# Kernel optimization log

Hardware: AMD Instinct MI355X
Metric: run time of the kernel (lower is better)

Reference implementation:

```python
import jax, jax.numpy as jnp
import numpy as np

B, T, D_IN, H, S, DH = 128, 256, 512, 1024, 128, 1024

def _lin(key, out_d, in_d):
    k = 1.0 / np.sqrt(in_d)
    return jax.random.uniform(key, (out_d, in_d), jnp.float32, -k, k)

def setup_inputs() -> dict:
    key = jax.random.key(0)
    ks = jax.random.split(key, 16)
    kH = 1.0 / np.sqrt(H)
    return {
        'x': jax.random.normal(ks[0], (B, T, D_IN), jnp.float32),
        'noise': jax.random.normal(ks[1], (B, T, S), jnp.float32),
        # LSTM (torch gate order: i, f, g, o)
        'W_ih': _lin(ks[2], 4 * H, S),
        'W_hh': _lin(ks[3], 4 * H, H),
        'b_ih': jax.random.uniform(ks[4], (4 * H,), jnp.float32, -kH, kH),
        'b_hh': jax.random.uniform(ks[5], (4 * H,), jnp.float32, -kH, kH),
        # posterior heads over concat(x_t, h_t): in = H + D_IN
        'Wm': _lin(ks[6], S, H + D_IN), 'bm': jnp.zeros((S,), jnp.float32),
        'Wv': _lin(ks[7], S, H + D_IN), 'bv': jnp.zeros((S,), jnp.float32),
        # decoder MLP
        'Wd1': _lin(ks[8], DH, S), 'bd1': jnp.zeros((DH,), jnp.float32),
        'Wd2': _lin(ks[9], D_IN, DH), 'bd2': jnp.zeros((D_IN,), jnp.float32),
    }

def reference(x, noise, W_ih, W_hh, b_ih, b_hh, Wm, bm, Wv, bv, Wd1, bd1, Wd2, bd2):
    Bb = x.shape[0]
    Hh = W_hh.shape[1]
    Ss = Wm.shape[0]
    dt = x.dtype

    def step(carry, inp):
        h, c, z = carry          # [B,H], [B,H], [B,S]
        xt, nt = inp             # [B,D_IN], [B,S]
        gates = z @ W_ih.T + b_ih + h @ W_hh.T + b_hh   # [B,4H]
        i, f, g, o = jnp.split(gates, 4, axis=-1)
        c = jax.nn.sigmoid(f) * c + jax.nn.sigmoid(i) * jnp.tanh(g)
        h = jax.nn.sigmoid(o) * jnp.tanh(c)
        pi = jnp.concatenate([xt, h], axis=-1)           # [B, D_IN+H]
        mean = pi @ Wm.T + bm
        log_var = pi @ Wv.T + bv
        std = jnp.exp(0.5 * log_var)
        z_new = nt * std + mean
        kl = jnp.sum(std * std + mean * mean - jnp.log(std) - 0.5)
        return (h, c, z_new), (z_new, kl)

    init = (jnp.zeros((Bb, Hh), dt), jnp.zeros((Bb, Hh), dt), jnp.zeros((Bb, Ss), dt))
    xs = (jnp.swapaxes(x, 0, 1), jnp.swapaxes(noise, 0, 1))  # time-major
    _, (zs, kls) = jax.lax.scan(step, init, xs)
    z = jnp.swapaxes(zs, 0, 1)                                # [B,T,S]
    kl = jnp.sum(kls)
    x_hat = jax.nn.relu(z @ Wd1.T + bd1) @ Wd2.T + bd2        # [B,T,D_IN]
    return x_hat, kl
```

## Files before the change

### kernel.cpp

```cpp
#include <hip/hip_runtime.h>
#include <hip/hip_bf16.h>

#define Bdim 128
#define Tdim 256
#define DIN 512
#define Hdim 1024
#define Sdim 128
#define DHdim 1024
#define KG 1152
#define KP 1536
#define NBLK 192

using short8  = __attribute__((ext_vector_type(8))) short;
using floatx4 = __attribute__((ext_vector_type(4))) float;
typedef unsigned long long ull;

#define MFMA(a, b, c) __builtin_amdgcn_mfma_f32_16x16x32_bf16((a), (b), (c), 0, 0, 0)

#define XBF_OFF   0ull
#define WG_OFF    33554432ull
#define WMV_OFF   42991616ull
#define HB_OFF    0ull
#define WD1_OFF   67108864ull
#define WD2_OFF   67371008ull
#define AB_OFF    68419584ull
#define AB_SZ     294912ull
#define ZALL_OFF  69009408ull
#define KL_OFF    77398016ull
#define FLG_OFF   77398144ull

__device__ __forceinline__ float sigf(float v) { return 1.0f / (1.0f + __expf(-v)); }
__device__ __forceinline__ float tanhfast(float v) { return 1.0f - 2.0f / (__expf(2.0f * v) + 1.0f); }

__device__ __forceinline__ short8 cload16(const __hip_bfloat16* p) {
  short8 r;
  asm volatile("global_load_dwordx4 %0, %1, off sc0 sc1" : "=&v"(r) : "v"(p));
  return r;
}
#define VMWAIT0()                                              \
  do {                                                         \
    asm volatile("s_waitcnt vmcnt(0)" ::: "memory");           \
    __builtin_amdgcn_sched_barrier(0);                         \
  } while (0)
#define CFENCE() asm volatile("" ::: "memory")

__device__ __forceinline__ void astore8(__hip_bfloat16* p, ull v) {
  __hip_atomic_store((ull*)(void*)p, v, __ATOMIC_RELAXED, __HIP_MEMORY_SCOPE_AGENT);
}

__device__ __forceinline__ void waitflags(unsigned* flags, int base, int mask,
                                          unsigned target, int lane) {
  unsigned* p = flags + base + (lane & mask);
  while (!__all((int)(__hip_atomic_load(p, __ATOMIC_RELAXED, __HIP_MEMORY_SCOPE_AGENT) >= target))) {
    __builtin_amdgcn_s_sleep(8);
  }
}

__global__ __launch_bounds__(256) void prep_kernel(
    const float* __restrict__ x, const float* __restrict__ W_ih,
    const float* __restrict__ W_hh, const float* __restrict__ Wm,
    const float* __restrict__ Wv, const float* __restrict__ Wd1,
    const float* __restrict__ Wd2, char* __restrict__ ws) {
  long long i = (long long)blockIdx.x * 256 + threadIdx.x;
  if (i < 16777216LL) {
    ((__hip_bfloat16*)(ws + XBF_OFF))[i] = __float2bfloat16(x[i]);
    return;
  }
  i -= 16777216LL;
  if (i < 4718592LL) {
    int j = (int)(i / KG), k = (int)(i % KG);
    float v = (k < Sdim) ? W_ih[j * Sdim + k] : W_hh[(long long)j * Hdim + (k - Sdim)];
    ((__hip_bfloat16*)(ws + WG_OFF))[i] = __float2bfloat16(v);
    return;
  }
  i -= 4718592LL;
  if (i < 393216LL) {
    int r = (int)(i / KP), k = (int)(i % KP);
    float v = (r < Sdim) ? Wm[r * KP + k] : Wv[(r - Sdim) * KP + k];
    ((__hip_bfloat16*)(ws + WMV_OFF))[i] = __float2bfloat16(v);
    return;
  }
  i -= 393216LL;
  if (i < 131072LL) { ((__hip_bfloat16*)(ws + WD1_OFF))[i] = __float2bfloat16(Wd1[i]); return; }
  i -= 131072LL;
  if (i < 524288LL) { ((__hip_bfloat16*)(ws + WD2_OFF))[i] = __float2bfloat16(Wd2[i]); return; }
  i -= 524288LL;
  if (i < 147456LL) { ((__hip_bfloat16*)(ws + AB_OFF))[i] = __float2bfloat16(0.0f); return; }
  i -= 147456LL;
  if (i == 0) { *((float*)(ws + KL_OFF)) = 0.0f; return; }
  i -= 1;
  if (i < 192LL) { ((unsigned*)(ws + FLG_OFF))[i] = 0u; return; }
}

__global__ __launch_bounds__(256, 1) void scan_kernel(
    char* __restrict__ ws, const float* __restrict__ noise,
    const float* __restrict__ b_ih, const float* __restrict__ b_hh,
    const float* __restrict__ bm, const float* __restrict__ bv) {
  const __hip_bfloat16* WG = (const __hip_bfloat16*)(ws + WG_OFF);
  const __hip_bfloat16* WMV = (const __hip_bfloat16*)(ws + WMV_OFF);
  const __hip_bfloat16* xbf = (const __hip_bfloat16*)(ws + XBF_OFF);
  __hip_bfloat16* zall = (__hip_bfloat16*)(ws + ZALL_OFF);
  float* klacc = (float*)(ws + KL_OFF);
  unsigned* flags = (unsigned*)(ws + FLG_OFF);

  __shared__ float smem[8 * 256];

  const int tid = threadIdx.x;
  const int lane = tid & 63;
  const int w = tid >> 6;
  const int row16 = lane & 15;
  const int quad = lane >> 4;
  const bool is_gates = (blockIdx.x < 128);

  const __hip_bfloat16* gb_bp[4];
  float biasv[4];
  int mhalf = 0, ngrp = 0;
  float creg[4] = {0.f, 0.f, 0.f, 0.f};
  const __hip_bfloat16* hd_bpm = nullptr;
  const __hip_bfloat16* hd_bpv = nullptr;
  int hd_mb = 0, hd_sb = 0, hd_nx = 0, hd_kbase = 0;
  float hbm = 0.f, hbv = 0.f;
  float klw = 0.f;

  if (is_gates) {
    mhalf = blockIdx.x >> 6;
    ngrp = blockIdx.x & 63;
    #pragma unroll
    for (int j = 0; j < 4; j++) {
      int idx = j * Hdim + ngrp * 16 + row16;
      gb_bp[j] = WG + (size_t)idx * KG;
      biasv[j] = b_ih[idx] + b_hh[idx];
    }
  } else {
    int hb = blockIdx.x - 128;
    hd_mb = hb >> 3;
    hd_sb = hb & 7;
    int s = hd_sb * 16 + row16;
    hd_bpm = WMV + (size_t)s * KP;
    hd_bpv = WMV + (size_t)(128 + s) * KP;
    hbm = bm[s];
    hbv = bv[s];
    hd_kbase = w * 384;
    hd_nx = (hd_kbase < DIN) ? ((DIN - hd_kbase) >> 5) : 0;
    if (hd_nx > 12) hd_nx = 12;
  }

  for (int t = 0; t < Tdim; t++) {
    const int par = t & 1;
    const __hip_bfloat16* Ab = (const __hip_bfloat16*)(ws + AB_OFF + (ull)par * AB_SZ);
    __hip_bfloat16* AbW = (__hip_bfloat16*)(ws + AB_OFF + (ull)(par ^ 1) * AB_SZ);

    if (is_gates) {
      const __hip_bfloat16* aptr = Ab + (size_t)(mhalf * 64 + w * 16 + row16) * KG;
      floatx4 acc[4];
      #pragma unroll
      for (int j = 0; j < 4; j++)
        acc[j] = (floatx4){biasv[j], biasv[j], biasv[j], biasv[j]};

      if (w == 0) waitflags(flags, mhalf * 64, 63, (unsigned)t, lane);
      __syncthreads();
      short8 areg[32];
      #pragma unroll
      for (int kt = 0; kt < 32; kt++)
        areg[kt] = cload16(aptr + Sdim + kt * 32 + quad * 8);
      VMWAIT0();
      #pragma unroll
      for (int kt = 0; kt < 32; kt++) {
        int k0 = Sdim + kt * 32 + quad * 8;
        #pragma unroll
        for (int j = 0; j < 4; j++)
          acc[j] = MFMA(areg[kt], *(const short8*)(gb_bp[j] + k0), acc[j]);
      }
      if (w == 0) waitflags(flags, 128 + mhalf * 32, 31, (unsigned)t, lane);
      __syncthreads();
      short8 zreg[4];
      #pragma unroll
      for (int kt = 0; kt < 4; kt++)
        zreg[kt] = cload16(aptr + kt * 32 + quad * 8);
      VMWAIT0();
      #pragma unroll
      for (int kt = 0; kt < 4; kt++) {
        int k0 = kt * 32 + quad * 8;
        #pragma unroll
        for (int j = 0; j < 4; j++)
          acc[j] = MFMA(zreg[kt], *(const short8*)(gb_bp[j] + k0), acc[j]);
      }
      int hc = ngrp * 16 + row16;
      #pragma unroll
      for (int r = 0; r < 4; r++) {
        float cn = sigf(acc[1][r]) * creg[r] + sigf(acc[0][r]) * tanhfast(acc[2][r]);
        creg[r] = cn;
        float hn = sigf(acc[3][r]) * tanhfast(cn);
        __hip_bfloat16 hbf = __float2bfloat16(hn);
        unsigned hu = (unsigned)reinterpret_cast<unsigned short&>(hbf);
        unsigned up = hu | (__shfl_xor(hu, 1, 64) << 16);
        unsigned uq = __shfl_xor(up, 2, 64);
        if ((row16 & 3) == 0) {
          int grow = mhalf * 64 + w * 16 + quad * 4 + r;
          astore8(AbW + (size_t)grow * KG + Sdim + hc, (ull)up | ((ull)uq << 32));
        }
      }
      __syncthreads();
      if (tid == 0)
        __hip_atomic_store(&flags[blockIdx.x], (unsigned)(t + 1),
                           __ATOMIC_RELAXED, __HIP_MEMORY_SCOPE_AGENT);
    } else {
      float nz[4];
      if (w == 0) {
        #pragma unroll
        for (int r = 0; r < 4; r++) {
          int b = hd_mb * 16 + quad * 4 + r;
          int s = hd_sb * 16 + row16;
          nz[r] = noise[((size_t)b * Tdim + t) * Sdim + s];
        }
      }
      const __hip_bfloat16* axp = xbf + ((size_t)(hd_mb * 16 + row16) * Tdim + t) * DIN;
      const __hip_bfloat16* ahp = AbW + (size_t)(hd_mb * 16 + row16) * KG + Sdim;
      floatx4 am, av;
      if (w == 0) { am = (floatx4){hbm, hbm, hbm, hbm}; av = (floatx4){hbv, hbv, hbv, hbv}; }
      else        { am = (floatx4){0.f, 0.f, 0.f, 0.f}; av = (floatx4){0.f, 0.f, 0.f, 0.f}; }
      #pragma unroll
      for (int kt = 0; kt < 12; kt++) {
        if (kt < hd_nx) {
          int k0 = hd_kbase + kt * 32 + quad * 8;
          short8 a = *(const short8*)(axp + k0);
          am = MFMA(a, *(const short8*)(hd_bpm + k0), am);
          av = MFMA(a, *(const short8*)(hd_bpv + k0), av);
        }
      }
      if (w == 0) waitflags(flags, (hd_mb >> 2) * 64, 63, (unsigned)(t + 1), lane);
      __syncthreads();
      short8 hreg[12];
      #pragma unroll
      for (int kt = 0; kt < 12; kt++) {
        if (kt >= hd_nx)
          hreg[kt] = cload16(ahp + hd_kbase + kt * 32 + quad * 8 - DIN);
      }
      VMWAIT0();
      #pragma unroll
      for (int kt = 0; kt < 12; kt++) {
        if (kt >= hd_nx) {
          int k0 = hd_kbase + kt * 32 + quad * 8;
          am = MFMA(hreg[kt], *(const short8*)(hd_bpm + k0), am);
          av = MFMA(hreg[kt], *(const short8*)(hd_bpv + k0), av);
        }
      }
      #pragma unroll
      for (int r = 0; r < 4; r++) {
        smem[(w * 2 + 0) * 256 + lane * 4 + r] = am[r];
        smem[(w * 2 + 1) * 256 + lane * 4 + r] = av[r];
      }
      __syncthreads();
      if (w == 0) {
        #pragma unroll
        for (int r = 0; r < 4; r++) {
          int idx = lane * 4 + r;
          float mean = smem[0 * 256 + idx] + smem[2 * 256 + idx] +
                       smem[4 * 256 + idx] + smem[6 * 256 + idx];
          float lv = smem[1 * 256 + idx] + smem[3 * 256 + idx] +
                     smem[5 * 256 + idx] + smem[7 * 256 + idx];
          int b = hd_mb * 16 + quad * 4 + r;
          int s = hd_sb * 16 + row16;
          float std = __expf(0.5f * lv);
          float z = nz[r] * std + mean;
          __hip_bfloat16 zb = __float2bfloat16(z);
          zall[((size_t)b * Tdim + t) * Sdim + s] = zb;
          unsigned zu = (unsigned)reinterpret_cast<unsigned short&>(zb);
          unsigned up = zu | (__shfl_xor(zu, 1, 64) << 16);
          unsigned uq = __shfl_xor(up, 2, 64);
          if ((row16 & 3) == 0)
            astore8(AbW + (size_t)b * KG + s, (ull)up | ((ull)uq << 32));
          klw += std * std + mean * mean - 0.5f * lv - 0.5f;
        }
      }
      __syncthreads();
      if (tid == 0)
        __hip_atomic_store(&flags[blockIdx.x], (unsigned)(t + 1),
                           __ATOMIC_RELAXED, __HIP_MEMORY_SCOPE_AGENT);
    }
  }
  if (!is_gates && w == 0) {
    #pragma unroll
    for (int off = 32; off > 0; off >>= 1) klw += __shfl_down(klw, off, 64);
    if (lane == 0) atomicAdd(klacc, klw);
  }
}

__global__ __launch_bounds__(256) void dec1_kernel(char* __restrict__ ws,
                                                   const float* __restrict__ bd1) {
  const __hip_bfloat16* zall = (const __hip_bfloat16*)(ws + ZALL_OFF);
  const __hip_bfloat16* Wd1b = (const __hip_bfloat16*)(ws + WD1_OFF);
  __hip_bfloat16* Hbuf = (__hip_bfloat16*)(ws + HB_OFF);
  int tid = threadIdx.x, lane = tid & 63, w = tid >> 6;
  int mb = blockIdx.x, nb = blockIdx.y;
  int row16 = lane & 15, quad = lane >> 4;
  int arow = mb * 64 + w * 16 + row16;
  const __hip_bfloat16* aptr = zall + (size_t)arow * Sdim;
  floatx4 acc[4] = {{0.f,0.f,0.f,0.f},{0.f,0.f,0.f,0.f},{0.f,0.f,0.f,0.f},{0.f,0.f,0.f,0.f}};
  #pragma unroll
  for (int kt = 0; kt < Sdim / 32; kt++) {
    int k0 = kt * 32 + quad * 8;
    short8 a = *(const short8*)(aptr + k0);
    #pragma unroll
    for (int j = 0; j < 4; j++) {
      const __hip_bfloat16* bp = Wd1b + (size_t)(nb * 64 + j * 16 + row16) * Sdim;
      acc[j] = MFMA(a, *(const short8*)(bp + k0), acc[j]);
    }
  }
  #pragma unroll
  for (int j = 0; j < 4; j++) {
    int n = nb * 64 + j * 16 + row16;
    float bias = bd1[n];
    #pragma unroll
    for (int r = 0; r < 4; r++) {
      int rr = mb * 64 + w * 16 + quad * 4 + r;
      float v = fmaxf(acc[j][r] + bias, 0.0f);
      Hbuf[(size_t)rr * DHdim + n] = __float2bfloat16(v);
    }
  }
}

__global__ __launch_bounds__(256) void dec2_kernel(char* __restrict__ ws,
                                                   const float* __restrict__ bd2,
                                                   float* __restrict__ out) {
  const __hip_bfloat16* Hbuf = (const __hip_bfloat16*)(ws + HB_OFF);
  const __hip_bfloat16* Wd2b = (const __hip_bfloat16*)(ws + WD2_OFF);
  int tid = threadIdx.x, lane = tid & 63, w = tid >> 6;
  int mb = blockIdx.x, nb = blockIdx.y;
  int row16 = lane & 15, quad = lane >> 4;
  int arow = mb * 64 + w * 16 + row16;
  const __hip_bfloat16* aptr = Hbuf + (size_t)arow * DHdim;
  const __hip_bfloat16* bp[4];
  #pragma unroll
  for (int j = 0; j < 4; j++) bp[j] = Wd2b + (size_t)(nb * 64 + j * 16 + row16) * DHdim;
  floatx4 acc[4] = {{0.f,0.f,0.f,0.f},{0.f,0.f,0.f,0.f},{0.f,0.f,0.f,0.f},{0.f,0.f,0.f,0.f}};
  for (int kt = 0; kt < DHdim / 32; kt++) {
    int k0 = kt * 32 + quad * 8;
    short8 a = *(const short8*)(aptr + k0);
    #pragma unroll
    for (int j = 0; j < 4; j++)
      acc[j] = MFMA(a, *(const short8*)(bp[j] + k0), acc[j]);
  }
  #pragma unroll
  for (int j = 0; j < 4; j++) {
    int n = nb * 64 + j * 16 + row16;
    float bias = bd2[n];
    #pragma unroll
    for (int r = 0; r < 4; r++) {
      int rr = mb * 64 + w * 16 + quad * 4 + r;
      out[(size_t)rr * DIN + n] = acc[j][r] + bias;
    }
  }
}

__global__ void kl_write_kernel(const char* __restrict__ ws, float* __restrict__ out) {
  if (threadIdx.x == 0 && blockIdx.x == 0)
    out[16777216] = *(const float*)(ws + KL_OFF);
}

extern "C" void kernel_launch(void* const* d_in, const int* in_sizes, int n_in,
                              void* d_out, int out_size, void* d_ws, size_t ws_size,
                              hipStream_t stream) {
  const float* x = (const float*)d_in[0];
  const float* noise = (const float*)d_in[1];
  const float* W_ih = (const float*)d_in[2];
  const float* W_hh = (const float*)d_in[3];
  const float* b_ih = (const float*)d_in[4];
  const float* b_hh = (const float*)d_in[5];
  const float* Wm = (const float*)d_in[6];
  const float* bm = (const float*)d_in[7];
  const float* Wv = (const float*)d_in[8];
  const float* bv = (const float*)d_in[9];
  const float* Wd1 = (const float*)d_in[10];
  const float* bd1 = (const float*)d_in[11];
  const float* Wd2 = (const float*)d_in[12];
  const float* bd2 = (const float*)d_in[13];
  char* ws = (char*)d_ws;
  float* out = (float*)d_out;

  long long total_prep = 22692033LL;
  int pblocks = (int)((total_prep + 255) / 256);
  prep_kernel<<<pblocks, 256, 0, stream>>>(x, W_ih, W_hh, Wm, Wv, Wd1, Wd2, ws);
  scan_kernel<<<NBLK, 256, 0, stream>>>(ws, noise, b_ih, b_hh, bm, bv);
  dec1_kernel<<<dim3(512, 16), 256, 0, stream>>>(ws, bd1);
  dec2_kernel<<<dim3(512, 8), 256, 0, stream>>>(ws, bd2, out);
  kl_write_kernel<<<1, 64, 0, stream>>>(ws, out);
}
```

Baseline: 6.618 ms.

## Replicate recurrent state buffers eight ways to spread cross-block reads

The shared double-buffered h/z activation buffer becomes eight replicas in the workspace. Each block reads from its own replica, chosen by blockIdx mod 8, and every producer writes its h or z slice to all eight. The aim is to spread the per-step coherent reads that all 192 blocks issue across different memory and cache locations, likely to ease contention on one region across XCDs. In exchange every producer store is done eight times, which adds write traffic and latency on the serial timestep path, and prep must zero eight times as much buffer space.

```diff
diff --git a/kernel.cpp b/kernel.cpp
--- a/kernel.cpp
+++ b/kernel.cpp
@@ -10,6 +10,7 @@
 #define KG 1152
 #define KP 1536
 #define NBLK 192
+#define REPN 8
 
 using short8  = __attribute__((ext_vector_type(8))) short;
 using floatx4 = __attribute__((ext_vector_type(4))) float;
@@ -21,10 +22,11 @@
 #define WG_OFF    33554432ull
 #define WMV_OFF   42991616ull
 #define HB_OFF    0ull
+#define REP_OFF   43778048ull
+#define AB_SZ     294912ull
+#define ABPAIR    589824ull
 #define WD1_OFF   67108864ull
 #define WD2_OFF   67371008ull
-#define AB_OFF    68419584ull
-#define AB_SZ     294912ull
 #define ZALL_OFF  69009408ull
 #define KL_OFF    77398016ull
 #define FLG_OFF   77398144ull
@@ -42,7 +44,6 @@
     asm volatile("s_waitcnt vmcnt(0)" ::: "memory");           \
     __builtin_amdgcn_sched_barrier(0);                         \
   } while (0)
-#define CFENCE() asm volatile("" ::: "memory")
 
 __device__ __forceinline__ void astore8(__hip_bfloat16* p, ull v) {
   __hip_atomic_store((ull*)(void*)p, v, __ATOMIC_RELAXED, __HIP_MEMORY_SCOPE_AGENT);
@@ -85,8 +86,12 @@
   i -= 131072LL;
   if (i < 524288LL) { ((__hip_bfloat16*)(ws + WD2_OFF))[i] = __float2bfloat16(Wd2[i]); return; }
   i -= 524288LL;
-  if (i < 147456LL) { ((__hip_bfloat16*)(ws + AB_OFF))[i] = __float2bfloat16(0.0f); return; }
-  i -= 147456LL;
+  if (i < 1179648LL) {
+    int rep = (int)(i / 147456LL), off = (int)(i % 147456LL);
+    ((__hip_bfloat16*)(ws + REP_OFF + (ull)rep * ABPAIR))[off] = __float2bfloat16(0.0f);
+    return;
+  }
+  i -= 1179648LL;
   if (i == 0) { *((float*)(ws + KL_OFF)) = 0.0f; return; }
   i -= 1;
   if (i < 192LL) { ((unsigned*)(ws + FLG_OFF))[i] = 0u; return; }
@@ -122,9 +127,11 @@
   float hbm = 0.f, hbv = 0.f;
   float klw = 0.f;
 
+  int myrep;
   if (is_gates) {
     mhalf = blockIdx.x >> 6;
     ngrp = blockIdx.x & 63;
+    myrep = blockIdx.x & 7;
     #pragma unroll
     for (int j = 0; j < 4; j++) {
       int idx = j * Hdim + ngrp * 16 + row16;
@@ -133,6 +140,7 @@
     }
   } else {
     int hb = blockIdx.x - 128;
+    myrep = hb & 7;
     hd_mb = hb >> 3;
     hd_sb = hb & 7;
     int s = hd_sb * 16 + row16;
@@ -144,11 +152,12 @@
     hd_nx = (hd_kbase < DIN) ? ((DIN - hd_kbase) >> 5) : 0;
     if (hd_nx > 12) hd_nx = 12;
   }
+  char* mybase = ws + REP_OFF + (ull)myrep * ABPAIR;
 
   for (int t = 0; t < Tdim; t++) {
     const int par = t & 1;
-    const __hip_bfloat16* Ab = (const __hip_bfloat16*)(ws + AB_OFF + (ull)par * AB_SZ);
-    __hip_bfloat16* AbW = (__hip_bfloat16*)(ws + AB_OFF + (ull)(par ^ 1) * AB_SZ);
+    const ull wofs = (ull)(par ^ 1) * AB_SZ;
+    const __hip_bfloat16* Ab = (const __hip_bfloat16*)(mybase + (ull)par * AB_SZ);
 
     if (is_gates) {
       const __hip_bfloat16* aptr = Ab + (size_t)(mhalf * 64 + w * 16 + row16) * KG;
@@ -197,7 +206,11 @@
         unsigned uq = __shfl_xor(up, 2, 64);
         if ((row16 & 3) == 0) {
           int grow = mhalf * 64 + w * 16 + quad * 4 + r;
-          astore8(AbW + (size_t)grow * KG + Sdim + hc, (ull)up | ((ull)uq << 32));
+          ull v8 = (ull)up | ((ull)uq << 32);
+          ull eoff = (ull)grow * KG + Sdim + hc;
+          #pragma unroll
+          for (int rp = 0; rp < REPN; rp++)
+            astore8((__hip_bfloat16*)(ws + REP_OFF + (ull)rp * ABPAIR + wofs) + eoff, v8);
         }
       }
       __syncthreads();
@@ -215,7 +228,8 @@
         }
       }
       const __hip_bfloat16* axp = xbf + ((size_t)(hd_mb * 16 + row16) * Tdim + t) * DIN;
-      const __hip_bfloat16* ahp = AbW + (size_t)(hd_mb * 16 + row16) * KG + Sdim;
+      const __hip_bfloat16* ahp = (const __hip_bfloat16*)(mybase + wofs) +
+                                  (size_t)(hd_mb * 16 + row16) * KG + Sdim;
       floatx4 am, av;
       if (w == 0) { am = (floatx4){hbm, hbm, hbm, hbm}; av = (floatx4){hbv, hbv, hbv, hbv}; }
       else        { am = (floatx4){0.f, 0.f, 0.f, 0.f}; av = (floatx4){0.f, 0.f, 0.f, 0.f}; }
@@ -268,8 +282,13 @@
           unsigned zu = (unsigned)reinterpret_cast<unsigned short&>(zb);
           unsigned up = zu | (__shfl_xor(zu, 1, 64) << 16);
           unsigned uq = __shfl_xor(up, 2, 64);
-          if ((row16 & 3) == 0)
-            astore8(AbW + (size_t)b * KG + s, (ull)up | ((ull)uq << 32));
+          if ((row16 & 3) == 0) {
+            ull v8 = (ull)up | ((ull)uq << 32);
+            ull eoff = (ull)b * KG + s;
+            #pragma unroll
+            for (int rp = 0; rp < REPN; rp++)
+              astore8((__hip_bfloat16*)(ws + REP_OFF + (ull)rp * ABPAIR + wofs) + eoff, v8);
+          }
           klw += std * std + mean * mean - 0.5f * lv - 0.5f;
         }
       }
@@ -378,7 +397,7 @@
   char* ws = (char*)d_ws;
   float* out = (float*)d_out;
 
-  long long total_prep = 22692033LL;
+  long long total_prep = 23724225LL;
   int pblocks = (int)((total_prep + 255) / 256);
   prep_kernel<<<pblocks, 256, 0, stream>>>(x, W_ih, W_hh, Wm, Wv, Wd1, Wd2, ws);
   scan_kernel<<<NBLK, 256, 0, stream>>>(ws, noise, b_ih, b_hh, bm, bv);
```

Measured after the change: 6.984 ms. +5.5%, slower.
